# Optimization experiments

Hardware: AMD Instinct MI355X
Metric: run time of the kernel (lower is better)

Reference implementation:

```python
import jax, jax.numpy as jnp
import numpy as np

N_SRC = 50000; N_DST = 50000; E = 800000
IN_NODE = 128; IN_EDGE = 16; OUT_NODE = 64; OUT_EDGE = 16; H = 4
LEAKY_SLOPE = 0.01  # F.leaky_relu default used inside dgl EGATConv


def setup_inputs() -> dict:
    key = jax.random.key(0)
    ks = jax.random.split(key, 11)
    return dict(
        nfeats=jax.random.normal(ks[0], (N_SRC, IN_NODE), jnp.float32),
        dst_feats=jax.random.normal(ks[1], (N_DST, IN_NODE), jnp.float32),
        reward=jax.random.uniform(ks[2], (E,), jnp.float32),
        src=jax.random.randint(ks[3], (E,), 0, N_SRC),
        dst=jax.random.randint(ks[4], (E,), 0, N_DST),
        W_ns=jax.random.normal(ks[5], (IN_NODE, H * OUT_NODE), jnp.float32) * 0.05,
        b_ns=jnp.zeros((H * OUT_NODE,), jnp.float32),
        W_ni=jax.random.normal(ks[6], (IN_NODE, H * OUT_EDGE), jnp.float32) * 0.05,
        W_nj=jax.random.normal(ks[7], (IN_NODE, H * OUT_EDGE), jnp.float32) * 0.05,
        W_fij=jax.random.normal(ks[8], (IN_EDGE, H * OUT_EDGE), jnp.float32) * 0.05,
        attn=jax.random.normal(ks[9], (H, OUT_EDGE), jnp.float32) * 0.05,
        b_e=jnp.zeros((H * OUT_EDGE,), jnp.float32),
    )


def reference(nfeats, dst_feats, reward, src, dst,
              W_ns, b_ns, W_ni, W_nj, W_fij, attn, b_e):
    # EGAT.forward with num_layers=1: efeats = reward repeated to IN_EDGE cols
    efeats = jnp.repeat(reward[:, None], IN_EDGE, axis=1)              # (E, Fe_in)
    # --- EGATConv ---
    f_ni = nfeats @ W_ni                                               # (Ns, H*Fe)
    f_nj = dst_feats @ W_nj                                            # (Nd, H*Fe)
    f_out = f_ni[src] + f_nj[dst] + efeats @ W_fij + b_e               # (E, H*Fe)
    f_out = jax.nn.leaky_relu(f_out, LEAKY_SLOPE).reshape(E, H, OUT_EDGE)
    e = jnp.einsum('ehf,hf->eh', f_out, attn)                          # (E, H)
    # edge softmax over incoming edges of each dst node (stable)
    m = jax.ops.segment_max(e, dst, num_segments=N_DST)                # (Nd, H)
    a = jnp.exp(e - m[dst])
    s = jax.ops.segment_sum(a, dst, num_segments=N_DST)                # (Nd, H)
    a = a / jnp.where(s > 0, s, 1.0)[dst]                              # (E, H)
    # weighted aggregation of projected src features
    h_src = (nfeats @ W_ns + b_ns).reshape(N_SRC, H, OUT_NODE)
    msg = h_src[src] * a[:, :, None]                                   # (E, H, Fn)
    h_out = jax.ops.segment_sum(msg, dst, num_segments=N_DST)          # (Nd, H, Fn)
    # wrapper: mean over heads then ReLU
    return jax.nn.relu(h_out.mean(axis=1))                             # (Nd, Fn)
```

## Files before the change

kernel.cpp:

```cpp
#include <hip/hip_runtime.h>

#define IN_NODE 128
#define OUT_NODE 64
#define NHEAD 4
#define HN 256
#define HE 64
#define LEAKY 0.01f

typedef __attribute__((ext_vector_type(8))) short bf16x8;
typedef __attribute__((ext_vector_type(4))) float f32x4;
typedef __attribute__((ext_vector_type(2))) float f32x2;

__device__ __forceinline__ float bf2f(unsigned short u) {
    union { unsigned u; float f; } v; v.u = ((unsigned)u) << 16; return v.f;
}
__device__ __forceinline__ unsigned short f2bf(float x) {
    union { float f; unsigned u; } v; v.f = x;
    unsigned r = v.u + 0x7FFF + ((v.u >> 16) & 1);
    return (unsigned short)(r >> 16);
}
__device__ __forceinline__ bf16x8 cvt8(float4 a, float4 b) {
    bf16x8 r;
    r[0] = (short)f2bf(a.x); r[1] = (short)f2bf(a.y);
    r[2] = (short)f2bf(a.z); r[3] = (short)f2bf(a.w);
    r[4] = (short)f2bf(b.x); r[5] = (short)f2bf(b.y);
    r[6] = (short)f2bf(b.z); r[7] = (short)f2bf(b.w);
    return r;
}
__device__ __forceinline__ f32x2 bfcvt2(unsigned d) {
    union { unsigned u; float f; } lo, hi;
    lo.u = d << 16; hi.u = d & 0xFFFF0000u;
    f32x2 r; r.x = lo.f; r.y = hi.f; return r;
}

__global__ void prep_w(const float* __restrict__ W_fij,
                       const float* __restrict__ W_ni,
                       const float* __restrict__ W_ns,
                       const float* __restrict__ W_nj,
                       float* __restrict__ wsum, unsigned short* __restrict__ WT) {
    int b = blockIdx.x;
    if (b == 0) {
        int k = threadIdx.x;
        if (k < 64) {
            float s = 0.f;
#pragma unroll
            for (int c = 0; c < 16; ++c) s += W_fij[c * 64 + k];
            wsum[k] = s;
        }
        return;
    }
    int base = (b - 1) * 4096 + threadIdx.x;
#pragma unroll
    for (int i = 0; i < 16; ++i) {
        int idx = base + i * 256;
        int g   = idx >> 11;
        int rem = idx & 2047;
        int c   = rem >> 9;
        int l   = (rem >> 3) & 63;
        int j   = rem & 7;
        int nl  = l & 15;
        int k   = c * 32 + (l >> 4) * 8 + j;
        unsigned short v;
        if (g < 4)       v = f2bf(W_ni[k * 64  + g * 16 + nl]);
        else if (g < 20) v = f2bf(W_ns[k * 256 + (g - 4) * 16 + nl]);
        else             v = f2bf(W_nj[k * 64  + (g - 20) * 16 + nl]);
        WT[idx] = v;
    }
}

__global__ __launch_bounds__(256) void scan_all(const int* __restrict__ cnt,
                                                int* __restrict__ row_ptr,
                                                int* __restrict__ partials,
                                                int* __restrict__ flags,
                                                int n, int E, int nb) {
    __shared__ int sums[256];
    __shared__ int s_base;
    int tid = threadIdx.x, b = blockIdx.x;
    int base = b * 1024;
    int v[4]; int tsum = 0;
#pragma unroll
    for (int j = 0; j < 4; ++j) {
        int idx = base + tid * 4 + j;
        v[j] = (idx < n) ? cnt[idx] : 0;
        tsum += v[j];
    }
    sums[tid] = tsum;
    __syncthreads();
    for (int off = 1; off < 256; off <<= 1) {
        int x = (tid >= off) ? sums[tid - off] : 0;
        __syncthreads();
        sums[tid] += x;
        __syncthreads();
    }
    if (tid == 255) {
        __hip_atomic_store(&partials[b], sums[255], __ATOMIC_RELAXED, __HIP_MEMORY_SCOPE_AGENT);
        __hip_atomic_store(&flags[b], 1, __ATOMIC_RELEASE, __HIP_MEMORY_SCOPE_AGENT);
    }
    if (tid < 64) {
        int val = 0;
        if (tid < nb) {
            while (__hip_atomic_load(&flags[tid], __ATOMIC_ACQUIRE, __HIP_MEMORY_SCOPE_AGENT) == 0) {
                __builtin_amdgcn_s_sleep(1);
            }
            val = __hip_atomic_load(&partials[tid], __ATOMIC_RELAXED, __HIP_MEMORY_SCOPE_AGENT);
        }
#pragma unroll
        for (int o = 1; o < 64; o <<= 1) {
            int x = __shfl_up(val, o);
            if (tid >= o) val += x;
        }
        int off = (b > 0) ? __shfl(val, b - 1) : 0;
        if (tid == 0) s_base = off;
    }
    __syncthreads();
    int run = s_base + sums[tid] - tsum;
#pragma unroll
    for (int j = 0; j < 4; ++j) {
        int idx = base + tid * 4 + j;
        if (idx < n) row_ptr[idx] = run;
        run += v[j];
    }
    if (b == nb - 1 && tid == 0) row_ptr[n] = E;
}

template<int NG, int G0>
__device__ __forceinline__ void gemm_tile(
    const float* __restrict__ A, int rowBase, int M,
    const unsigned short* __restrict__ WB, const float* __restrict__ b_ns,
    unsigned short* __restrict__ f_ni, unsigned short* __restrict__ h_src,
    unsigned short* __restrict__ f_nj, unsigned short* As)
{
    const int t = threadIdx.x;
    const float4* A4 = reinterpret_cast<const float4*>(A);
#pragma unroll
    for (int j = 0; j < 4; ++j) {
        int gi = j * 256 + t;
        int r  = gi >> 4;
        int gr = rowBase + r; if (gr >= M) gr = M - 1;
        int fi = (gi & 15) * 2;
        float4 a0 = A4[(size_t)gr * 32 + fi];
        float4 a1 = A4[(size_t)gr * 32 + fi + 1];
        int byteoff = (gi * 16) ^ ((r & 7) << 4);
        *reinterpret_cast<bf16x8*>(reinterpret_cast<char*>(As) + byteoff) = cvt8(a0, a1);
    }
    __syncthreads();

    const int lane = t & 63, w = t >> 6;
    const int rw = rowBase + w * 16;
    if (rw >= M) return;
    const int m = lane & 15, q = lane >> 4;
    const int tr = w * 16 + m;

    f32x4 acc[NG] = {};
    const char* Asb = reinterpret_cast<const char*>(As);
#pragma unroll
    for (int c = 0; c < 4; ++c) {
        int gi  = tr * 16 + c * 4 + q;
        int off = (gi * 16) ^ ((tr & 7) << 4);
        bf16x8 af = *reinterpret_cast<const bf16x8*>(Asb + off);
#pragma unroll
        for (int g = 0; g < NG; ++g) {
            bf16x8 bf = *reinterpret_cast<const bf16x8*>(
                WB + (size_t)(((G0 + g) * 4 + c) * 64 + lane) * 8);
            acc[g] = __builtin_amdgcn_mfma_f32_16x16x32_bf16(af, bf, acc[g], 0, 0, 0);
        }
    }

#pragma unroll
    for (int g = 0; g < NG; ++g) {
        const int ga = G0 + g;
        unsigned short* C; int N, colBase; const float* bias = nullptr;
        if (ga < 4)       { C = f_ni;  N = 64;  colBase = ga * 16; }
        else if (ga < 20) { C = h_src; N = 256; colBase = (ga - 4) * 16; bias = b_ns; }
        else              { C = f_nj;  N = 64;  colBase = (ga - 20) * 16; }
        int col = colBase + m;
        float bv = bias ? bias[col] : 0.f;
#pragma unroll
        for (int rr = 0; rr < 4; ++rr) {
            int orow = rw + q * 4 + rr;
            if (orow < M) C[(size_t)orow * N + col] = f2bf(acc[g][rr] + bv);
        }
    }
}

__global__ __launch_bounds__(256) void hist_gemm(
    const float* __restrict__ nfeats, const float* __restrict__ dst_feats,
    const unsigned short* __restrict__ WT, const float* __restrict__ b_ns,
    const int* __restrict__ dst,
    int* __restrict__ cnt, int* __restrict__ rank,
    unsigned short* __restrict__ f_ni, unsigned short* __restrict__ h_src,
    unsigned short* __restrict__ f_nj,
    int Ns, int Nd, int E, int nBlkNf, int nBlkDj)
{
    __shared__ __align__(16) unsigned short As[64 * 128];
    const int g = blockIdx.x >> 1, r = blockIdx.x & 1;
    if (r == 1) {
        if (g < 2 * nBlkNf) {
            int tile = g >> 1;
            if ((g & 1) == 0)
                gemm_tile<10, 0>(nfeats, tile * 64, Ns, WT, b_ns, f_ni, h_src, f_nj, As);
            else
                gemm_tile<10, 10>(nfeats, tile * 64, Ns, WT, b_ns, f_ni, h_src, f_nj, As);
        } else if (g < 2 * nBlkNf + nBlkDj) {
            gemm_tile<4, 20>(dst_feats, (g - 2 * nBlkNf) * 64, Nd, WT, b_ns, f_ni, h_src, f_nj, As);
        }
        return;
    }
    int i = g * 256 + threadIdx.x;
    if (i < E) rank[i] = atomicAdd(&cnt[dst[i]], 1);
}

__global__ __launch_bounds__(256) void scatter_k(
    const int* __restrict__ src, const int* __restrict__ dst,
    const float* __restrict__ reward, const int* __restrict__ row_ptr,
    const int* __restrict__ rank, int2* __restrict__ sr_s, int E)
{
    int i = blockIdx.x * 256 + threadIdx.x;
    if (i >= E) return;
    int d = dst[i];
    sr_s[row_ptr[d] + rank[i]] = make_int2(src[i], __float_as_int(reward[i]));
}

struct G { uint2 ui; uint4 h0; uint4 h1; };
__device__ __forceinline__ G gatherE(const unsigned short* __restrict__ f_ni,
                                     const unsigned short* __restrict__ h_src,
                                     int sn, int ll, int hq) {
    G g;
    g.ui = *reinterpret_cast<const uint2*>(f_ni + (size_t)sn * HE + 4 * ll);
    const unsigned short* hp = h_src + (size_t)sn * HN + hq;
    g.h0 = *reinterpret_cast<const uint4*>(hp);
    g.h1 = *reinterpret_cast<const uint4*>(hp + 8);
    return g;
}

__global__ __launch_bounds__(256) void fused_agg(
    const unsigned short* __restrict__ f_ni, const unsigned short* __restrict__ f_nj,
    const unsigned short* __restrict__ h_src, const int2* __restrict__ sr_s,
    const int* __restrict__ row_ptr,
    const float* __restrict__ wsum, const float* __restrict__ b_e,
    const float* __restrict__ attn, float* __restrict__ out, int Nd)
{
    __shared__ float red[4][1024];
    const int wv = threadIdx.x >> 6, lane = threadIdx.x & 63;
    const int d = blockIdx.x * 4 + wv;
    if (d >= Nd) return;
    const int ll = lane & 15, sub = lane >> 4;
    const int hq = ((lane >> 2) & 3) * 64 + (lane & 3) * 16;
    const int mql = (lane >> 1) & 3;

    float4 wsv = *reinterpret_cast<const float4*>(wsum + 4 * ll);
    float4 bev = *reinterpret_cast<const float4*>(b_e + 4 * ll);
    float4 atv = *reinterpret_cast<const float4*>(attn + 4 * ll);
    f32x2 ws01 = {wsv.x, wsv.y}, ws23 = {wsv.z, wsv.w};
    f32x2 at01 = {atv.x, atv.y}, at23 = {atv.z, atv.w};
    const f32x2 lk2 = {LEAKY, LEAKY};

    const int beg = row_ptr[d];
    const int end = row_ptr[d + 1];
    const int deg = end - beg;

    float den = 0.f;
    f32x2 a0 = {}, a1 = {}, a2 = {}, a3 = {}, a4 = {}, a5 = {}, a6 = {}, a7 = {};

    if (deg > 0) {
        uint2 uj = *reinterpret_cast<const uint2*>(f_nj + (size_t)d * HE + 4 * ll);
        f32x2 bb01 = bfcvt2(uj.x) + (f32x2){bev.x, bev.y};
        f32x2 bb23 = bfcvt2(uj.y) + (f32x2){bev.z, bev.w};
        const int nq = (deg + 3) >> 2;
        const int last = end - 1;

#define LDSR(q) ({ int qq_ = ((q) < nq) ? (q) : (nq - 1);                 \
                   int slot_ = beg + qq_ * 4 + sub;                       \
                   if (slot_ > last) slot_ = last;                        \
                   sr_s[slot_]; })

#define COMPUTE(sr, gg, kq) do {                                          \
    float r_ = __int_as_float((sr).y);                                    \
    f32x2 r2_ = {r_, r_};                                                 \
    f32x2 v01_ = bfcvt2((gg).ui.x) + r2_ * ws01 + bb01;                   \
    f32x2 v23_ = bfcvt2((gg).ui.y) + r2_ * ws23 + bb23;                   \
    v01_ = __builtin_elementwise_max(v01_, v01_ * lk2);                   \
    v23_ = __builtin_elementwise_max(v23_, v23_ * lk2);                   \
    f32x2 t2_ = v01_ * at01 + v23_ * at23;                                \
    float t_ = t2_.x + t2_.y;                                             \
    t_ += __shfl_xor(t_, 1);                                              \
    t_ += __shfl_xor(t_, 2);                                              \
    float ev_ = ((beg + (kq) * 4 + sub) < end) ? __expf(t_) : 0.f;        \
    den += ev_;                                                           \
    f32x2 ev2_ = {ev_, ev_};                                              \
    a0 += bfcvt2((gg).h0.x) * ev2_;                                       \
    a1 += bfcvt2((gg).h0.y) * ev2_;                                       \
    a2 += bfcvt2((gg).h0.z) * ev2_;                                       \
    a3 += bfcvt2((gg).h0.w) * ev2_;                                       \
    a4 += bfcvt2((gg).h1.x) * ev2_;                                       \
    a5 += bfcvt2((gg).h1.y) * ev2_;                                       \
    a6 += bfcvt2((gg).h1.z) * ev2_;                                       \
    a7 += bfcvt2((gg).h1.w) * ev2_;                                       \
} while (0)

        int2 sr0 = LDSR(0), sr1 = LDSR(1);
        G gA = gatherE(f_ni, h_src, sr0.x, ll, hq);
        for (int k = 0; k < nq; ++k) {
            int2 sr2 = LDSR(k + 2);
            G gB = gatherE(f_ni, h_src, sr1.x, ll, hq);
            COMPUTE(sr0, gA, k);
            sr0 = sr1; sr1 = sr2; gA = gB;
        }
#undef COMPUTE
#undef LDSR
    }

    den += __shfl_xor(den, 16);
    den += __shfl_xor(den, 32);
    float sc = (den > 0.f) ? 0.25f / den : 0.f;
    float* wr = &red[wv][lane * 16];
    float4 s0 = {a0.x * sc, a0.y * sc, a1.x * sc, a1.y * sc};
    float4 s1 = {a2.x * sc, a2.y * sc, a3.x * sc, a3.y * sc};
    float4 s2 = {a4.x * sc, a4.y * sc, a5.x * sc, a5.y * sc};
    float4 s3 = {a6.x * sc, a6.y * sc, a7.x * sc, a7.y * sc};
    *reinterpret_cast<float4*>(wr + ((0 ^ mql) << 2)) = s0;
    *reinterpret_cast<float4*>(wr + ((1 ^ mql) << 2)) = s1;
    *reinterpret_cast<float4*>(wr + ((2 ^ mql) << 2)) = s2;
    *reinterpret_cast<float4*>(wr + ((3 ^ mql) << 2)) = s3;
    asm volatile("s_waitcnt lgkmcnt(0)" ::: "memory");
    float ssum = 0.f;
    const int e = lane & 15, c45 = lane >> 4;
#pragma unroll
    for (int s = 0; s < 4; ++s)
#pragma unroll
        for (int h = 0; h < 4; ++h) {
            int L = s * 16 + h * 4 + c45;
            int m2 = (L >> 1) & 3;
            int fi = L * 16 + (((e >> 2) ^ m2) << 2) + (e & 3);
            ssum += red[wv][fi];
        }
    out[(size_t)d * OUT_NODE + lane] = fmaxf(ssum, 0.f);
}

static inline char* align256(char* p) {
    return (char*)(((uintptr_t)p + 255) & ~(uintptr_t)255);
}

extern "C" void kernel_launch(void* const* d_in, const int* in_sizes, int n_in,
                              void* d_out, int out_size, void* d_ws, size_t ws_size,
                              hipStream_t stream) {
    const float* nfeats    = (const float*)d_in[0];
    const float* dst_feats = (const float*)d_in[1];
    const float* reward    = (const float*)d_in[2];
    const int*   src       = (const int*)d_in[3];
    const int*   dst       = (const int*)d_in[4];
    const float* W_ns      = (const float*)d_in[5];
    const float* b_ns      = (const float*)d_in[6];
    const float* W_ni      = (const float*)d_in[7];
    const float* W_nj      = (const float*)d_in[8];
    const float* W_fij     = (const float*)d_in[9];
    const float* attn      = (const float*)d_in[10];
    const float* b_e       = (const float*)d_in[11];
    float* out = (float*)d_out;

    const int Ns = in_sizes[0] / IN_NODE;
    const int Nd = in_sizes[1] / IN_NODE;
    const int E  = in_sizes[2];

    char* ws = (char*)d_ws;
    unsigned short* f_ni  = (unsigned short*)ws; ws = align256(ws + (size_t)Ns * HE * 2);
    unsigned short* f_nj  = (unsigned short*)ws; ws = align256(ws + (size_t)Nd * HE * 2);
    unsigned short* h_src = (unsigned short*)ws; ws = align256(ws + (size_t)Ns * HN * 2);
    unsigned short* WT    = (unsigned short*)ws; ws = align256(ws + 49152 * 2);
    float* wsum    = (float*)ws; ws = align256(ws + HE * 4);
    int*   cnt     = (int*)ws;
    int*   flags   = cnt + Nd;   ws = align256(ws + (size_t)(Nd + 64) * 4);
    int*   row_ptr = (int*)ws;   ws = align256(ws + (size_t)(Nd + 1) * 4);
    int*   partials= (int*)ws;   ws = align256(ws + 256 * 4);
    int2*  sr_s    = (int2*)ws;  ws = align256(ws + (size_t)E * 8);
    int*   rank    = (int*)ws;   ws = align256(ws + (size_t)E * 4);

    hipMemsetAsync(cnt, 0, (size_t)(Nd + 64) * 4, stream);

    prep_w<<<13, 256, 0, stream>>>(W_fij, W_ni, W_ns, W_nj, wsum, WT);

    int nBlkNf = (Ns + 63) / 64;
    int nBlkDj = (Nd + 63) / 64;
    int nU = 2 * nBlkNf + nBlkDj;
    int nHist = (E + 255) / 256;
    int nGroups = (nHist > nU) ? nHist : nU;
    hist_gemm<<<nGroups * 2, 256, 0, stream>>>(
        nfeats, dst_feats, WT, b_ns, dst, cnt, rank,
        f_ni, h_src, f_nj, Ns, Nd, E, nBlkNf, nBlkDj);

    int nb = (Nd + 1023) / 1024;
    scan_all<<<nb, 256, 0, stream>>>(cnt, row_ptr, partials, flags, Nd, E, nb);

    scatter_k<<<(E + 255) / 256, 256, 0, stream>>>(
        src, dst, reward, row_ptr, rank, sr_s, E);

    fused_agg<<<(Nd + 3) / 4, 256, 0, stream>>>(
        f_ni, f_nj, h_src, sr_s, row_ptr, wsum, b_e, attn, out, Nd);
}
```

Measured before the change: 259.6 us.

## Split GEMM tiles across histogram and scatter kernels for better overlap

The node-projection GEMM tiles were previously all co-scheduled with the destination histogram kernel. This change splits the GEMM units in half, running the first half alongside the histogram and the second half alongside the edge scatter. The aim is to balance work between the two launches and hide the scatter's memory latency behind compute. The scatter kernel gains LDS usage and paired block indexing, which may lower its occupancy.

New measurement: 253.1 us. -2.5%, faster.

```diff
diff --git a/kernel.cpp b/kernel.cpp
--- a/kernel.cpp
+++ b/kernel.cpp
@@ -183,6 +183,24 @@
     }
 }
 
+__device__ __forceinline__ void gemm_unit(
+    int u, const float* __restrict__ nfeats, const float* __restrict__ dst_feats,
+    const unsigned short* __restrict__ WT, const float* __restrict__ b_ns,
+    unsigned short* __restrict__ f_ni, unsigned short* __restrict__ h_src,
+    unsigned short* __restrict__ f_nj, unsigned short* As,
+    int Ns, int Nd, int nBlkNf, int nBlkDj)
+{
+    if (u < 2 * nBlkNf) {
+        int tile = u >> 1;
+        if ((u & 1) == 0)
+            gemm_tile<10, 0>(nfeats, tile * 64, Ns, WT, b_ns, f_ni, h_src, f_nj, As);
+        else
+            gemm_tile<10, 10>(nfeats, tile * 64, Ns, WT, b_ns, f_ni, h_src, f_nj, As);
+    } else if (u < 2 * nBlkNf + nBlkDj) {
+        gemm_tile<4, 20>(dst_feats, (u - 2 * nBlkNf) * 64, Nd, WT, b_ns, f_ni, h_src, f_nj, As);
+    }
+}
+
 __global__ __launch_bounds__(256) void hist_gemm(
     const float* __restrict__ nfeats, const float* __restrict__ dst_feats,
     const unsigned short* __restrict__ WT, const float* __restrict__ b_ns,
@@ -190,32 +208,41 @@
     int* __restrict__ cnt, int* __restrict__ rank,
     unsigned short* __restrict__ f_ni, unsigned short* __restrict__ h_src,
     unsigned short* __restrict__ f_nj,
-    int Ns, int Nd, int E, int nBlkNf, int nBlkDj)
+    int Ns, int Nd, int E, int nBlkNf, int nBlkDj, int u0, int u1)
 {
     __shared__ __align__(16) unsigned short As[64 * 128];
     const int g = blockIdx.x >> 1, r = blockIdx.x & 1;
     if (r == 1) {
-        if (g < 2 * nBlkNf) {
-            int tile = g >> 1;
-            if ((g & 1) == 0)
-                gemm_tile<10, 0>(nfeats, tile * 64, Ns, WT, b_ns, f_ni, h_src, f_nj, As);
-            else
-                gemm_tile<10, 10>(nfeats, tile * 64, Ns, WT, b_ns, f_ni, h_src, f_nj, As);
-        } else if (g < 2 * nBlkNf + nBlkDj) {
-            gemm_tile<4, 20>(dst_feats, (g - 2 * nBlkNf) * 64, Nd, WT, b_ns, f_ni, h_src, f_nj, As);
-        }
+        int u = u0 + g;
+        if (u < u1)
+            gemm_unit(u, nfeats, dst_feats, WT, b_ns, f_ni, h_src, f_nj, As,
+                      Ns, Nd, nBlkNf, nBlkDj);
         return;
     }
     int i = g * 256 + threadIdx.x;
     if (i < E) rank[i] = atomicAdd(&cnt[dst[i]], 1);
 }
 
-__global__ __launch_bounds__(256) void scatter_k(
+__global__ __launch_bounds__(256) void scat_gemm(
+    const float* __restrict__ nfeats, const float* __restrict__ dst_feats,
+    const unsigned short* __restrict__ WT, const float* __restrict__ b_ns,
     const int* __restrict__ src, const int* __restrict__ dst,
     const float* __restrict__ reward, const int* __restrict__ row_ptr,
-    const int* __restrict__ rank, int2* __restrict__ sr_s, int E)
+    const int* __restrict__ rank, int2* __restrict__ sr_s,
+    unsigned short* __restrict__ f_ni, unsigned short* __restrict__ h_src,
+    unsigned short* __restrict__ f_nj,
+    int Ns, int Nd, int E, int nBlkNf, int nBlkDj, int u0, int u1)
 {
-    int i = blockIdx.x * 256 + threadIdx.x;
+    __shared__ __align__(16) unsigned short As[64 * 128];
+    const int g = blockIdx.x >> 1, r = blockIdx.x & 1;
+    if (r == 1) {
+        int u = u0 + g;
+        if (u < u1)
+            gemm_unit(u, nfeats, dst_feats, WT, b_ns, f_ni, h_src, f_nj, As,
+                      Ns, Nd, nBlkNf, nBlkDj);
+        return;
+    }
+    int i = g * 256 + threadIdx.x;
     if (i >= E) return;
     int d = dst[i];
     sr_s[row_ptr[d] + rank[i]] = make_int2(src[i], __float_as_int(reward[i]));
@@ -381,18 +408,23 @@
 
     int nBlkNf = (Ns + 63) / 64;
     int nBlkDj = (Nd + 63) / 64;
-    int nU = 2 * nBlkNf + nBlkDj;
-    int nHist = (E + 255) / 256;
-    int nGroups = (nHist > nU) ? nHist : nU;
-    hist_gemm<<<nGroups * 2, 256, 0, stream>>>(
+    int nU  = 2 * nBlkNf + nBlkDj;
+    int nUA = (nU + 1) / 2;
+    int nE256 = (E + 255) / 256;
+
+    int g1 = (nE256 > nUA) ? nE256 : nUA;
+    hist_gemm<<<g1 * 2, 256, 0, stream>>>(
         nfeats, dst_feats, WT, b_ns, dst, cnt, rank,
-        f_ni, h_src, f_nj, Ns, Nd, E, nBlkNf, nBlkDj);
+        f_ni, h_src, f_nj, Ns, Nd, E, nBlkNf, nBlkDj, 0, nUA);
 
     int nb = (Nd + 1023) / 1024;
     scan_all<<<nb, 256, 0, stream>>>(cnt, row_ptr, partials, flags, Nd, E, nb);
 
-    scatter_k<<<(E + 255) / 256, 256, 0, stream>>>(
-        src, dst, reward, row_ptr, rank, sr_s, E);
+    int nUB = nU - nUA;
+    int g3 = (nE256 > nUB) ? nE256 : nUB;
+    scat_gemm<<<g3 * 2, 256, 0, stream>>>(
+        nfeats, dst_feats, WT, b_ns, src, dst, reward, row_ptr, rank, sr_s,
+        f_ni, h_src, f_nj, Ns, Nd, E, nBlkNf, nBlkDj, nUA, nU);
 
     fused_agg<<<(Nd + 3) / 4, 256, 0, stream>>>(
         f_ni, f_nj, h_src, sr_s, row_ptr, wsum, b_e, attn, out, Nd);
```
